# Optimization experiments

Measured on AMD Instinct MI355X. Metric: run time of the kernel, lower is better.

## Reference

```python
import jax, jax.numpy as jnp
import numpy as np

SELECTED_CLASS = 1  # matches init_kwargs


def _edt_sq(mask):
    """Exact squared Euclidean distance of each pixel to the nearest False pixel.
    Matches scipy.ndimage.distance_transform_edt(mask)**2 (2-pass separable,
    column scan + exact row-wise parabola minimization done brute-force in chunks).
    mask: (H, W) bool.
    """
    H, W = mask.shape
    BIG = np.float32(H + W)  # > any possible true distance, safe sentinel
    g = np.where(mask, BIG, np.float32(0.0)).astype(np.float32)
    for i in range(1, H):
        np.minimum(g[i], g[i - 1] + 1, out=g[i])
    for i in range(H - 2, -1, -1):
        np.minimum(g[i], g[i + 1] + 1, out=g[i])
    g2 = g * g  # (H, W) squared column distances
    k = np.arange(W, dtype=np.float32)
    d2 = np.empty((H, W), np.float32)
    CH = 64  # chunk of output columns to bound temp memory
    for j0 in range(0, W, CH):
        j = k[j0:j0 + CH]
        diff2 = (j[None, :] - k[:, None]) ** 2  # (W, Jc)
        d2[:, j0:j0 + CH] = (g2[:, :, None] + diff2[None]).min(axis=1)
    return d2


def _inner_boundary(mask):
    """skimage.segmentation.find_boundaries(mask, mode='inner'), connectivity=1:
    foreground pixels with at least one in-image 4-neighbor in background."""
    p = np.pad(mask, 1, constant_values=True)
    ero = p[1:-1, :-2] & p[1:-1, 2:] & p[:-2, 1:-1] & p[2:, 1:-1] & mask
    return mask & ~ero


def compute_sdf_np(y_true_sel):
    """Normalized signed distance map, faithful to BoundaryLoss.compute_sdf.
    y_true_sel: (B, 1, H, W) float; returns (B, 1, H, W) float32 in [-1, 1]."""
    masks = y_true_sel[:, 0].astype(bool)
    B, H, W = masks.shape
    out = np.zeros((B, 1, H, W), np.float32)
    for b in range(B):
        m = masks[b]
        if not m.any():
            continue  # original leaves zeros
        posdis = np.sqrt(_edt_sq(m))
        negdis = np.sqrt(_edt_sq(~m))
        sdf = (negdis - negdis.min()) / (negdis.max() - negdis.min()) \
            - (posdis - posdis.min()) / (posdis.max() - posdis.min())
        sdf[_inner_boundary(m)] = 0.0
        out[b, 0] = sdf
    return out


def setup_inputs():
    key = jax.random.key(0)
    k1, k2 = jax.random.split(key)
    B, C, H, W = 8, 4, 512, 512
    y_pred = jax.random.normal(k1, (B, C, H, W), dtype=jnp.float32)
    y_true = jax.random.randint(k2, (B, C, H, W), 0, 2).astype(jnp.float32)
    return {"y_pred": y_pred, "y_true": y_true}


def reference(y_pred, y_true):
    sel = SELECTED_CLASS
    # GT signed distance map (host-side, non-differentiable, as in the original
    # which round-trips through scipy on CPU): shape (B, 1, H, W)
    gt_sdf = jnp.asarray(compute_sdf_np(np.asarray(y_true[:, sel:sel + 1])))
    pc = jax.nn.sigmoid(y_pred)  # (B, C, H, W)
    # torch.einsum('bchw,bchw->bchw', pc, dc) with dc having c=1 broadcasts over C
    mult = pc * gt_sdf
    return mult.mean(axis=(1, 2, 3)).mean()
```

## Files before the change

kernel.cpp:

```cpp
#include <hip/hip_runtime.h>
#include <math.h>

#define B 8
#define C 4
#define H 512
#define W 512
#define SEL 1
#define BIGI 1024
#define NPIX (B*H*W)
#define CH 64
#define RC 8
#define TC 32
#define NSEG 16
#define LL 4
#define CINF 3000
#define G 4

__global__ __launch_bounds__(512) void col_two_level(const float* __restrict__ ytrue,
                                                     unsigned short* __restrict__ gpk,
                                                     unsigned* __restrict__ sumsD,
                                                     unsigned* __restrict__ sumsU) {
    __shared__ int sP[NSEG][TC + 1], sN[NSEG][TC + 1];
    __shared__ int sCP[NSEG][TC + 1], sCN[NSEG][TC + 1];

    int blk = blockIdx.x;
    int b   = blk >> 7;
    int rem = blk & 127;
    int jt  = rem >> 3;
    int rc  = rem & 7;
    int tid = threadIdx.x;
    int tx  = tid & (TC - 1);
    int ty  = tid >> 5;
    int j   = jt * TC + tx;
    int i0  = rc * CH + ty * LL;

    const float* m = ytrue + ((size_t)b * C + SEL) * H * W + j;
    int gfp[LL], gfn[LL];
    int pp = BIGI, pn = BIGI;
    #pragma unroll
    for (int r = 0; r < LL; ++r) {
        bool fg = (m[(size_t)(i0 + r) * W] != 0.0f);
        int vp = fg ? BIGI : 0;
        int vn = fg ? 0 : BIGI;
        vp = min(vp, pp + 1); gfp[r] = vp; pp = vp;
        vn = min(vn, pn + 1); gfn[r] = vn; pn = vn;
    }
    sP[ty][tx] = pp - ty * LL;
    sN[ty][tx] = pn - ty * LL;
    __syncthreads();

    int col = tid >> 4, seg = tid & 15;
    int wp = sP[seg][col], wn = sN[seg][col];
    #pragma unroll
    for (int d = 1; d < NSEG; d <<= 1) {
        int up = __shfl_up(wp, d, 16);
        int un = __shfl_up(wn, d, 16);
        if (seg >= d) { wp = min(wp, up); wn = min(wn, un); }
    }
    if (seg < NSEG - 1) {
        sCP[seg + 1][col] = seg * LL + wp;
        sCN[seg + 1][col] = seg * LL + wn;
    } else {
        int jj = jt * TC + col;
        sumsD[((size_t)(b * RC + rc)) * W + jj] =
            (unsigned)(seg * LL + wp) | ((unsigned)(seg * LL + wn) << 16);
    }
    if (seg == 0) { sCP[0][col] = BIGI; sCN[0][col] = BIGI; }
    __syncthreads();

    int cp = sCP[ty][tx], cn = sCN[ty][tx];
    int lbp = 1 << 20, lbn = 1 << 20;
    #pragma unroll
    for (int r = 0; r < LL; ++r) {
        int vp = min(gfp[r], cp + 1 + r); gfp[r] = vp; lbp = min(lbp, vp + r);
        int vn = min(gfn[r], cn + 1 + r); gfn[r] = vn; lbn = min(lbn, vn + r);
    }
    sP[ty][tx] = lbp + ty * LL;
    sN[ty][tx] = lbn + ty * LL;
    __syncthreads();

    int w2p = sP[seg][col], w2n = sN[seg][col];
    #pragma unroll
    for (int d = 1; d < NSEG; d <<= 1) {
        int up = __shfl_down(w2p, d, 16);
        int un = __shfl_down(w2n, d, 16);
        if (seg + d < NSEG) { w2p = min(w2p, up); w2n = min(w2n, un); }
    }
    if (seg > 0) {
        sCP[seg - 1][col] = w2p - seg * LL;
        sCN[seg - 1][col] = w2n - seg * LL;
    } else {
        int jj = jt * TC + col;
        sumsU[((size_t)(b * RC + rc)) * W + jj] =
            (unsigned)w2p | ((unsigned)w2n << 16);
    }
    if (seg == NSEG - 1) { sCP[NSEG - 1][col] = BIGI; sCN[NSEG - 1][col] = BIGI; }
    __syncthreads();

    int pbp = sCP[ty][tx], pbn = sCN[ty][tx];
    unsigned short* op = gpk + ((size_t)b * H + i0) * W + j;
    #pragma unroll
    for (int r = LL - 1; r >= 0; --r) {
        int vp = min(gfp[r], pbp + 1); pbp = vp;
        int vn = min(gfn[r], pbn + 1); pbn = vn;
        int fg = (vn == 0) ? 1 : 0;
        int g  = vp + vn;
        op[(size_t)r * W] = (unsigned short)((g << 1) | fg);
    }
}

__global__ __launch_bounds__(512) void row_fused(const unsigned short* __restrict__ gpk,
                                                 const unsigned* __restrict__ sumsD,
                                                 const unsigned* __restrict__ sumsU,
                                                 const float* __restrict__ ypred,
                                                 float* __restrict__ rowpart) {
    __shared__ float2 s2[G][W];
    __shared__ float sw[4][8];

    int blk = blockIdx.x;
    int b = blk >> 7;
    int g = blk & 127;
    int i0 = g * G;
    int rc = i0 >> 6;
    int j = threadIdx.x;

    int Ap = CINF, An = CINF, Bp = CINF, Bn = CINF;
    #pragma unroll
    for (int q = 0; q < RC; ++q) {
        if (q < rc) {
            unsigned dv = sumsD[((size_t)(b * RC + q)) * W + j];
            int e = q * CH + CH - 1;
            Ap = min(Ap, (int)(dv & 0xFFFFu) - e);
            An = min(An, (int)(dv >> 16) - e);
        } else if (q > rc) {
            unsigned uv = sumsU[((size_t)(b * RC + q)) * W + j];
            int s0 = q * CH;
            Bp = min(Bp, (int)(uv & 0xFFFFu) + s0);
            Bn = min(Bn, (int)(uv >> 16) + s0);
        }
    }

    #pragma unroll
    for (int r = 0; r < G; ++r) {
        int ii = i0 + r;
        unsigned v = gpk[((size_t)b * H + ii) * W + j];
        int fg = v & 1;
        int gv = v >> 1;
        int gp = fg ? gv : 0;
        int gn = fg ? 0 : gv;
        gp = min(gp, min(Ap + ii, Bp - ii));
        gn = min(gn, min(An + ii, Bn - ii));
        s2[r][j] = make_float2((float)(gp * gp), (float)(gn * gn));
    }
    __syncthreads();

    float mxp = 0.f, mxn = 0.f, A = 0.f, Bv = 0.f;
    #pragma unroll
    for (int r = 0; r < G; ++r) {
        float2 v0 = s2[r][j];
        float bp = v0.x, bn = v0.y;
        for (int rr = 1; rr < W; ++rr) {
            float r2 = (float)(rr * rr);
            if (r2 >= bp && r2 >= bn) break;
            int jl = j - rr, jr = j + rr;
            if (jl >= 0) { float2 u = s2[r][jl]; bp = fminf(bp, u.x + r2); bn = fminf(bn, u.y + r2); }
            if (jr < W)  { float2 u = s2[r][jr]; bp = fminf(bp, u.x + r2); bn = fminf(bn, u.y + r2); }
        }
        float posdis = sqrtf(bp);
        float negdis = sqrtf(bn);
        bool bnd = (bp == 1.0f);

        const float* yp = ypred + ((size_t)b * C * H + i0 + r) * W + j;
        float s = 0.f;
        #pragma unroll
        for (int cc = 0; cc < C; ++cc) {
            float x = yp[(size_t)cc * H * W];
            s += 1.0f / (1.0f + __expf(-x));
        }
        float se = bnd ? 0.f : s;
        mxp = fmaxf(mxp, bp); mxn = fmaxf(mxn, bn);
        A += se * posdis; Bv += se * negdis;
    }

    for (int off = 32; off >= 1; off >>= 1) {
        mxp = fmaxf(mxp, __shfl_down(mxp, off));
        mxn = fmaxf(mxn, __shfl_down(mxn, off));
        A  += __shfl_down(A, off);
        Bv += __shfl_down(Bv, off);
    }
    int wave = threadIdx.x >> 6, lane = threadIdx.x & 63;
    if (lane == 0) { sw[0][wave] = mxp; sw[1][wave] = mxn; sw[2][wave] = A; sw[3][wave] = Bv; }
    __syncthreads();
    if (threadIdx.x == 0) {
        float a0 = sw[0][0], a1 = sw[1][0], a2 = sw[2][0], a3 = sw[3][0];
        #pragma unroll
        for (int w = 1; w < 8; ++w) {
            a0 = fmaxf(a0, sw[0][w]); a1 = fmaxf(a1, sw[1][w]);
            a2 += sw[2][w]; a3 += sw[3][w];
        }
        *(float4*)(rowpart + (size_t)blk * 4) = make_float4(a0, a1, a2, a3);
    }
}

__global__ __launch_bounds__(512) void batch_final(const float* __restrict__ rowpart,
                                                   float* __restrict__ out) {
    __shared__ double sacc[8];
    int bw = threadIdx.x >> 6;
    int lane = threadIdx.x & 63;
    const float4* rv = (const float4*)(rowpart + (size_t)bw * 128 * 4);
    float4 e0 = rv[lane];
    float4 e1 = rv[lane + 64];
    float mxp = fmaxf(e0.x, e1.x), mxn = fmaxf(e0.y, e1.y);
    float A = e0.z + e1.z, Bv = e0.w + e1.w;
    for (int off = 32; off >= 1; off >>= 1) {
        mxp = fmaxf(mxp, __shfl_down(mxp, off));
        mxn = fmaxf(mxn, __shfl_down(mxn, off));
        A  += __shfl_down(A, off);
        Bv += __shfl_down(Bv, off);
    }
    if (lane == 0) {
        float pmax = sqrtf(mxp), nmax = sqrtf(mxn);
        float invp = (pmax > 0.f) ? 1.0f / pmax : 0.0f;
        float invn = (nmax > 0.f) ? 1.0f / nmax : 0.0f;
        sacc[bw] = (pmax > 0.f) ? (double)(invn * Bv - invp * A) : 0.0;
    }
    __syncthreads();
    if (threadIdx.x == 0) {
        double tt = 0.0;
        #pragma unroll
        for (int q = 0; q < 8; ++q) tt += sacc[q];
        out[0] = (float)(tt / (double)((size_t)B * C * H * W));
    }
}

extern "C" void kernel_launch(void* const* d_in, const int* in_sizes, int n_in,
                              void* d_out, int out_size, void* d_ws, size_t ws_size,
                              hipStream_t stream) {
    const float* ypred = (const float*)d_in[0];
    const float* ytrue = (const float*)d_in[1];
    float* out = (float*)d_out;

    unsigned short* gpk = (unsigned short*)d_ws;
    unsigned* sumsD = (unsigned*)(gpk + NPIX);
    unsigned* sumsU = sumsD + (size_t)B * RC * W;
    float* rowpart = (float*)(sumsU + (size_t)B * RC * W);

    col_two_level<<<B * 16 * RC, 512, 0, stream>>>(ytrue, gpk, sumsD, sumsU);
    row_fused<<<B * H / G, W, 0, stream>>>(gpk, sumsD, sumsU, ypred, rowpart);
    batch_final<<<1, 512, 0, stream>>>(rowpart, out);
}
```

Baseline: 25.72 us.

## Fuse final reduction into row kernel and vectorize per-thread row work

Removes the separate batch_final launch. The row kernel now uses an atomic counter, reset by the column kernel, so the last block does the final reduction. The row kernel's thread mapping changes from one column across 4 rows to one row with 4 adjacent columns per thread, which lets the sums, gpk and ypred reads use vector loads. Launch bounds also request 4 blocks per CU. The cost is a per-block threadfence and atomic, plus possible load imbalance in the data-dependent parabola search, since each thread now handles 4 neighbouring pixels of a single row.

```diff
diff --git a/kernel.cpp b/kernel.cpp
--- a/kernel.cpp
+++ b/kernel.cpp
@@ -15,13 +15,17 @@
 #define LL 4
 #define CINF 3000
 #define G 4
+#define NRU (B*H/G)
 
 __global__ __launch_bounds__(512) void col_two_level(const float* __restrict__ ytrue,
                                                      unsigned short* __restrict__ gpk,
                                                      unsigned* __restrict__ sumsD,
-                                                     unsigned* __restrict__ sumsU) {
+                                                     unsigned* __restrict__ sumsU,
+                                                     unsigned* __restrict__ cnt) {
     __shared__ int sP[NSEG][TC + 1], sN[NSEG][TC + 1];
     __shared__ int sCP[NSEG][TC + 1], sCN[NSEG][TC + 1];
+
+    if (blockIdx.x == 0 && threadIdx.x == 0) *cnt = 0u;
 
     int blk = blockIdx.x;
     int b   = blk >> 7;
@@ -53,9 +57,9 @@
     int wp = sP[seg][col], wn = sN[seg][col];
     #pragma unroll
     for (int d = 1; d < NSEG; d <<= 1) {
-        int up = __shfl_up(wp, d, 16);
-        int un = __shfl_up(wn, d, 16);
-        if (seg >= d) { wp = min(wp, up); wn = min(wn, un); }
+        int a1 = __shfl_up(wp, d, 16);
+        int a2 = __shfl_up(wn, d, 16);
+        if (seg >= d) { wp = min(wp, a1); wn = min(wn, a2); }
     }
     if (seg < NSEG - 1) {
         sCP[seg + 1][col] = seg * LL + wp;
@@ -82,9 +86,9 @@
     int w2p = sP[seg][col], w2n = sN[seg][col];
     #pragma unroll
     for (int d = 1; d < NSEG; d <<= 1) {
-        int up = __shfl_down(w2p, d, 16);
-        int un = __shfl_down(w2n, d, 16);
-        if (seg + d < NSEG) { w2p = min(w2p, up); w2n = min(w2n, un); }
+        int a1 = __shfl_down(w2p, d, 16);
+        int a2 = __shfl_down(w2n, d, 16);
+        if (seg + d < NSEG) { w2p = min(w2p, a1); w2n = min(w2n, a2); }
     }
     if (seg > 0) {
         sCP[seg - 1][col] = w2p - seg * LL;
@@ -104,79 +108,104 @@
         int vp = min(gfp[r], pbp + 1); pbp = vp;
         int vn = min(gfn[r], pbn + 1); pbn = vn;
         int fg = (vn == 0) ? 1 : 0;
-        int g  = vp + vn;
-        op[(size_t)r * W] = (unsigned short)((g << 1) | fg);
+        int g2 = vp + vn;
+        op[(size_t)r * W] = (unsigned short)((g2 << 1) | fg);
     }
 }
 
-__global__ __launch_bounds__(512) void row_fused(const unsigned short* __restrict__ gpk,
-                                                 const unsigned* __restrict__ sumsD,
-                                                 const unsigned* __restrict__ sumsU,
-                                                 const float* __restrict__ ypred,
-                                                 float* __restrict__ rowpart) {
+__global__ __launch_bounds__(512, 4) void row_fused(const unsigned short* __restrict__ gpk,
+                                                    const unsigned* __restrict__ sumsD,
+                                                    const unsigned* __restrict__ sumsU,
+                                                    const float* __restrict__ ypred,
+                                                    float* __restrict__ rowpart,
+                                                    unsigned* __restrict__ cnt,
+                                                    float* __restrict__ out) {
     __shared__ float2 s2[G][W];
     __shared__ float sw[4][8];
+    __shared__ int lastFlag;
+    __shared__ double sacc[8];
 
     int blk = blockIdx.x;
     int b = blk >> 7;
     int g = blk & 127;
     int i0 = g * G;
     int rc = i0 >> 6;
-    int j = threadIdx.x;
-
-    int Ap = CINF, An = CINF, Bp = CINF, Bn = CINF;
-    #pragma unroll
-    for (int q = 0; q < RC; ++q) {
-        if (q < rc) {
-            unsigned dv = sumsD[((size_t)(b * RC + q)) * W + j];
-            int e = q * CH + CH - 1;
-            Ap = min(Ap, (int)(dv & 0xFFFFu) - e);
-            An = min(An, (int)(dv >> 16) - e);
-        } else if (q > rc) {
-            unsigned uv = sumsU[((size_t)(b * RC + q)) * W + j];
-            int s0 = q * CH;
-            Bp = min(Bp, (int)(uv & 0xFFFFu) + s0);
-            Bn = min(Bn, (int)(uv >> 16) + s0);
-        }
-    }
-
-    #pragma unroll
-    for (int r = 0; r < G; ++r) {
-        int ii = i0 + r;
-        unsigned v = gpk[((size_t)b * H + ii) * W + j];
-        int fg = v & 1;
-        int gv = v >> 1;
-        int gp = fg ? gv : 0;
-        int gn = fg ? 0 : gv;
-        gp = min(gp, min(Ap + ii, Bp - ii));
-        gn = min(gn, min(An + ii, Bn - ii));
-        s2[r][j] = make_float2((float)(gp * gp), (float)(gn * gn));
-    }
-    __syncthreads();
+    int tid = threadIdx.x;
+    int r = tid >> 7;
+    int q = tid & 127;
+    int j0 = q * 4;
+    int ii = i0 + r;
+
+    int Ap0 = CINF, Ap1 = CINF, Ap2 = CINF, Ap3 = CINF;
+    int An0 = CINF, An1 = CINF, An2 = CINF, An3 = CINF;
+    int Bp0 = CINF, Bp1 = CINF, Bp2 = CINF, Bp3 = CINF;
+    int Bn0 = CINF, Bn1 = CINF, Bn2 = CINF, Bn3 = CINF;
+    #pragma unroll
+    for (int qq = 0; qq < RC; ++qq) {
+        if (qq < rc) {
+            uint4 dv = *(const uint4*)(sumsD + ((size_t)(b * RC + qq)) * W + j0);
+            int e = qq * CH + CH - 1;
+            Ap0 = min(Ap0, (int)(dv.x & 0xFFFFu) - e); An0 = min(An0, (int)(dv.x >> 16) - e);
+            Ap1 = min(Ap1, (int)(dv.y & 0xFFFFu) - e); An1 = min(An1, (int)(dv.y >> 16) - e);
+            Ap2 = min(Ap2, (int)(dv.z & 0xFFFFu) - e); An2 = min(An2, (int)(dv.z >> 16) - e);
+            Ap3 = min(Ap3, (int)(dv.w & 0xFFFFu) - e); An3 = min(An3, (int)(dv.w >> 16) - e);
+        } else if (qq > rc) {
+            uint4 uv = *(const uint4*)(sumsU + ((size_t)(b * RC + qq)) * W + j0);
+            int s0 = qq * CH;
+            Bp0 = min(Bp0, (int)(uv.x & 0xFFFFu) + s0); Bn0 = min(Bn0, (int)(uv.x >> 16) + s0);
+            Bp1 = min(Bp1, (int)(uv.y & 0xFFFFu) + s0); Bn1 = min(Bn1, (int)(uv.y >> 16) + s0);
+            Bp2 = min(Bp2, (int)(uv.z & 0xFFFFu) + s0); Bn2 = min(Bn2, (int)(uv.z >> 16) + s0);
+            Bp3 = min(Bp3, (int)(uv.w & 0xFFFFu) + s0); Bn3 = min(Bn3, (int)(uv.w >> 16) + s0);
+        }
+    }
+
+    ushort4 gv4 = *(const ushort4*)(gpk + ((size_t)b * H + ii) * W + j0);
+    #define FIXPX(U, GV, AP, AN, BP, BN)                                          \
+        {                                                                         \
+            int fg = (int)(GV) & 1;                                               \
+            int gv = (int)(GV) >> 1;                                              \
+            int gp = fg ? gv : 0;                                                 \
+            int gn = fg ? 0 : gv;                                                 \
+            gp = min(gp, min((AP) + ii, (BP) - ii));                              \
+            gn = min(gn, min((AN) + ii, (BN) - ii));                              \
+            s2[r][j0 + U] = make_float2((float)(gp * gp), (float)(gn * gn));      \
+        }
+    FIXPX(0, gv4.x, Ap0, An0, Bp0, Bn0)
+    FIXPX(1, gv4.y, Ap1, An1, Bp1, Bn1)
+    FIXPX(2, gv4.z, Ap2, An2, Bp2, Bn2)
+    FIXPX(3, gv4.w, Ap3, An3, Bp3, Bn3)
+    #undef FIXPX
+    __syncthreads();
+
+    const float* yp = ypred + ((size_t)b * C * H + ii) * W + j0;
+    float4 y0 = *(const float4*)(yp);
+    float4 y1 = *(const float4*)(yp + (size_t)H * W);
+    float4 y2 = *(const float4*)(yp + (size_t)2 * H * W);
+    float4 y3 = *(const float4*)(yp + (size_t)3 * H * W);
 
     float mxp = 0.f, mxn = 0.f, A = 0.f, Bv = 0.f;
     #pragma unroll
-    for (int r = 0; r < G; ++r) {
+    for (int u = 0; u < 4; ++u) {
+        int j = j0 + u;
         float2 v0 = s2[r][j];
         float bp = v0.x, bn = v0.y;
         for (int rr = 1; rr < W; ++rr) {
             float r2 = (float)(rr * rr);
             if (r2 >= bp && r2 >= bn) break;
             int jl = j - rr, jr = j + rr;
-            if (jl >= 0) { float2 u = s2[r][jl]; bp = fminf(bp, u.x + r2); bn = fminf(bn, u.y + r2); }
-            if (jr < W)  { float2 u = s2[r][jr]; bp = fminf(bp, u.x + r2); bn = fminf(bn, u.y + r2); }
+            if (jl >= 0) { float2 uu = s2[r][jl]; bp = fminf(bp, uu.x + r2); bn = fminf(bn, uu.y + r2); }
+            if (jr < W)  { float2 uu = s2[r][jr]; bp = fminf(bp, uu.x + r2); bn = fminf(bn, uu.y + r2); }
         }
         float posdis = sqrtf(bp);
         float negdis = sqrtf(bn);
         bool bnd = (bp == 1.0f);
 
-        const float* yp = ypred + ((size_t)b * C * H + i0 + r) * W + j;
-        float s = 0.f;
-        #pragma unroll
-        for (int cc = 0; cc < C; ++cc) {
-            float x = yp[(size_t)cc * H * W];
-            s += 1.0f / (1.0f + __expf(-x));
-        }
+        float x0 = (u == 0) ? y0.x : (u == 1) ? y0.y : (u == 2) ? y0.z : y0.w;
+        float x1 = (u == 0) ? y1.x : (u == 1) ? y1.y : (u == 2) ? y1.z : y1.w;
+        float x2 = (u == 0) ? y2.x : (u == 1) ? y2.y : (u == 2) ? y2.z : y2.w;
+        float x3 = (u == 0) ? y3.x : (u == 1) ? y3.y : (u == 2) ? y3.z : y3.w;
+        float s = 1.0f / (1.0f + __expf(-x0)) + 1.0f / (1.0f + __expf(-x1))
+                + 1.0f / (1.0f + __expf(-x2)) + 1.0f / (1.0f + __expf(-x3));
         float se = bnd ? 0.f : s;
         mxp = fmaxf(mxp, bp); mxn = fmaxf(mxn, bn);
         A += se * posdis; Bv += se * negdis;
@@ -188,10 +217,10 @@
         A  += __shfl_down(A, off);
         Bv += __shfl_down(Bv, off);
     }
-    int wave = threadIdx.x >> 6, lane = threadIdx.x & 63;
+    int wave = tid >> 6, lane = tid & 63;
     if (lane == 0) { sw[0][wave] = mxp; sw[1][wave] = mxn; sw[2][wave] = A; sw[3][wave] = Bv; }
     __syncthreads();
-    if (threadIdx.x == 0) {
+    if (tid == 0) {
         float a0 = sw[0][0], a1 = sw[1][0], a2 = sw[2][0], a3 = sw[3][0];
         #pragma unroll
         for (int w = 1; w < 8; ++w) {
@@ -199,37 +228,39 @@
             a2 += sw[2][w]; a3 += sw[3][w];
         }
         *(float4*)(rowpart + (size_t)blk * 4) = make_float4(a0, a1, a2, a3);
-    }
-}
-
-__global__ __launch_bounds__(512) void batch_final(const float* __restrict__ rowpart,
-                                                   float* __restrict__ out) {
-    __shared__ double sacc[8];
-    int bw = threadIdx.x >> 6;
-    int lane = threadIdx.x & 63;
-    const float4* rv = (const float4*)(rowpart + (size_t)bw * 128 * 4);
-    float4 e0 = rv[lane];
-    float4 e1 = rv[lane + 64];
-    float mxp = fmaxf(e0.x, e1.x), mxn = fmaxf(e0.y, e1.y);
-    float A = e0.z + e1.z, Bv = e0.w + e1.w;
-    for (int off = 32; off >= 1; off >>= 1) {
-        mxp = fmaxf(mxp, __shfl_down(mxp, off));
-        mxn = fmaxf(mxn, __shfl_down(mxn, off));
-        A  += __shfl_down(A, off);
-        Bv += __shfl_down(Bv, off);
-    }
-    if (lane == 0) {
-        float pmax = sqrtf(mxp), nmax = sqrtf(mxn);
-        float invp = (pmax > 0.f) ? 1.0f / pmax : 0.0f;
-        float invn = (nmax > 0.f) ? 1.0f / nmax : 0.0f;
-        sacc[bw] = (pmax > 0.f) ? (double)(invn * Bv - invp * A) : 0.0;
-    }
-    __syncthreads();
-    if (threadIdx.x == 0) {
-        double tt = 0.0;
-        #pragma unroll
-        for (int q = 0; q < 8; ++q) tt += sacc[q];
-        out[0] = (float)(tt / (double)((size_t)B * C * H * W));
+        __threadfence();
+        unsigned prev = atomicAdd(cnt, 1u);
+        lastFlag = (prev == (unsigned)(NRU - 1)) ? 1 : 0;
+    }
+    __syncthreads();
+
+    if (lastFlag) {
+        __threadfence();
+        int bw = tid >> 6;
+        const float4* rv = (const float4*)(rowpart + (size_t)bw * 128 * 4);
+        float4 e0 = rv[lane];
+        float4 e1 = rv[lane + 64];
+        float fmxp = fmaxf(e0.x, e1.x), fmxn = fmaxf(e0.y, e1.y);
+        float fA = e0.z + e1.z, fBv = e0.w + e1.w;
+        for (int off = 32; off >= 1; off >>= 1) {
+            fmxp = fmaxf(fmxp, __shfl_down(fmxp, off));
+            fmxn = fmaxf(fmxn, __shfl_down(fmxn, off));
+            fA  += __shfl_down(fA, off);
+            fBv += __shfl_down(fBv, off);
+        }
+        if (lane == 0) {
+            float pmax = sqrtf(fmxp), nmax = sqrtf(fmxn);
+            float invp = (pmax > 0.f) ? 1.0f / pmax : 0.0f;
+            float invn = (nmax > 0.f) ? 1.0f / nmax : 0.0f;
+            sacc[bw] = (pmax > 0.f) ? (double)(invn * fBv - invp * fA) : 0.0;
+        }
+        __syncthreads();
+        if (tid == 0) {
+            double tt = 0.0;
+            #pragma unroll
+            for (int qb = 0; qb < 8; ++qb) tt += sacc[qb];
+            out[0] = (float)(tt / (double)((size_t)B * C * H * W));
+        }
     }
 }
 
@@ -244,8 +275,8 @@
     unsigned* sumsD = (unsigned*)(gpk + NPIX);
     unsigned* sumsU = sumsD + (size_t)B * RC * W;
     float* rowpart = (float*)(sumsU + (size_t)B * RC * W);
-
-    col_two_level<<<B * 16 * RC, 512, 0, stream>>>(ytrue, gpk, sumsD, sumsU);
-    row_fused<<<B * H / G, W, 0, stream>>>(gpk, sumsD, sumsU, ypred, rowpart);
-    batch_final<<<1, 512, 0, stream>>>(rowpart, out);
+    unsigned* cnt = (unsigned*)(rowpart + (size_t)NRU * 4);
+
+    col_two_level<<<B * 16 * RC, 512, 0, stream>>>(ytrue, gpk, sumsD, sumsU, cnt);
+    row_fused<<<NRU, 512, 0, stream>>>(gpk, sumsD, sumsU, ypred, rowpart, cnt, out);
 }
```

Measured after the change: 51.44 us. 2x slower.
